# Kernel tuning notes

Hardware: AMD Instinct MI355X
Metric: run time of the kernel (lower is better)

Reference implementation:

```python
import jax, jax.numpy as jnp
import numpy as np

N = 200          # fixed by map_norm's .view(200, 1)
D = 8192         # in_features
EPS = 1e-5


def setup_inputs() -> dict:
    key = jax.random.key(0)
    ks = jax.random.split(key, 7)
    lim = float(np.sqrt(6.0 / D))
    x = jax.random.normal(ks[0], (N, D), dtype=jnp.float32)
    Wq = jax.random.uniform(ks[1], (D, D), dtype=jnp.float32, minval=-lim, maxval=lim)
    Wk = jax.random.uniform(ks[2], (D, D), dtype=jnp.float32, minval=-lim, maxval=lim)
    Wv = jax.random.uniform(ks[3], (D, D), dtype=jnp.float32, minval=-lim, maxval=lim)
    bq = jax.random.normal(ks[4], (D,), dtype=jnp.float32) * 0.01
    bk = jax.random.normal(ks[5], (D,), dtype=jnp.float32) * 0.01
    bv = jax.random.normal(ks[6], (D,), dtype=jnp.float32) * 0.01
    return {"x": x, "Wq": Wq, "bq": bq, "Wk": Wk, "bk": bk, "Wv": Wv, "bv": bv}


def reference(x, Wq, bq, Wk, bk, Wv, bv):
    d_out = x.shape[1]
    cc = jnp.sqrt(jnp.asarray(d_out, dtype=x.dtype))
    # nn.Linear: y = x @ W.T + b
    q = x @ Wq.T + bq          # [N, D]
    k = x @ Wk.T + bk          # [N, D]
    v = x @ Wv.T + bv          # [N, D]
    s = q @ k.T                # [N, N] score map
    mean = jnp.mean(s, axis=-1, keepdims=True)
    var = jnp.var(s, axis=-1, keepdims=True, ddof=1)  # torch.var is unbiased
    s = (s - mean) / jnp.sqrt(var + EPS)
    s = jnp.sin(s)
    scores = jax.nn.softmax(s / cc, axis=-1)
    return scores @ v          # [N, D]
```

## Files before the change

kernel.cpp:

```cpp
#include <hip/hip_runtime.h>
#include <hip/hip_bf16.h>
#include <cstdint>

#define DD 8192
#define NROW 200
#define MT 13
#define MPAD 208
#define KPV 256
#define EPSV 1e-5f
#define BK 64
#define ABUF_BYTES (MPAD * BK * 2)

using short8 = __attribute__((ext_vector_type(8))) short;
using f32x4  = __attribute__((ext_vector_type(4))) float;

#define MEMBAR asm volatile("" ::: "memory")
#define RAWBAR asm volatile("s_barrier" ::: "memory")

__device__ __forceinline__ ushort f2bf(float f) {
    union { float f; unsigned u; } c; c.f = f;
    unsigned u = c.u;
    return (ushort)((u + 0x7FFFu + ((u >> 16) & 1u)) >> 16);
}

__device__ __forceinline__ short8 pack8(float4 a, float4 b) {
    short8 o;
    o[0]=f2bf(a.x); o[1]=f2bf(a.y); o[2]=f2bf(a.z); o[3]=f2bf(a.w);
    o[4]=f2bf(b.x); o[5]=f2bf(b.y); o[6]=f2bf(b.z); o[7]=f2bf(b.w);
    return o;
}

__global__ void cvt_x(const float* __restrict__ x, ushort* __restrict__ xb) {
    int i = (blockIdx.x * 256 + threadIdx.x) * 8;
    int row = i >> 13;
    int col = i & (DD - 1);
    short8 o;
    if (row < NROW) {
        const float4* p = reinterpret_cast<const float4*>(x + (size_t)row * DD + col);
        float4 a = p[0], b = p[1];
        o = pack8(a, b);
    } else {
        for (int j = 0; j < 8; ++j) o[j] = 0;
    }
    *reinterpret_cast<short8*>(xb + i) = o;
}

__global__ __launch_bounds__(128) void qkv_gemm(
    const ushort* __restrict__ xb,
    const float* __restrict__ Wq, const float* __restrict__ Wk, const float* __restrict__ Wv,
    const float* __restrict__ bq, const float* __restrict__ bk, const float* __restrict__ bv,
    ushort* __restrict__ qb, ushort* __restrict__ kb, ushort* __restrict__ vt)
{
    __shared__ char Asm[2 * ABUF_BYTES];

    const int mat = blockIdx.y;
    const float* W    = (mat == 0) ? Wq : (mat == 1 ? Wk : Wv);
    const float* bias = (mat == 0) ? bq : (mat == 1 ? bk : bv);

    const int t     = threadIdx.x;
    const int lane  = t & 63;
    const int wave  = t >> 6;
    const int col16 = lane & 15;
    const int kgrp  = lane >> 4;
    const int ncol  = blockIdx.x * 32 + wave * 16 + col16;

    const float* wp = W + (size_t)ncol * DD + kgrp * 8;

    const ushort* sbase = xb + (size_t)(t >> 3) * DD + (size_t)(((t & 7) ^ ((t >> 3) & 7)) * 8);
    char* dbase = Asm + wave * 1024;

    const int b0off = col16 * 128 + ((kgrp ^ (col16 & 7)) * 16);
    const int b1off = b0off ^ 64;

    f32x4 acc[MT];
    #pragma unroll
    for (int m = 0; m < MT; ++m)
        for (int r = 0; r < 4; ++r) acc[m][r] = 0.f;

#define STAGE(B, KK) { _Pragma("unroll") for (int r = 0; r < 13; ++r) { \
        __builtin_amdgcn_global_load_lds( \
            (const __attribute__((address_space(1))) void*)(sbase + (KK) + r * 16 * DD), \
            (__attribute__((address_space(3))) void*)(dbase + (B) * ABUF_BYTES + r * 2048), \
            16, 0, 0); } }

#define LOADW(d0, d1, d2, d3, KK) { \
        d0 = *reinterpret_cast<const float4*>(wp + (KK)); \
        d1 = *reinterpret_cast<const float4*>(wp + (KK) + 4); \
        d2 = *reinterpret_cast<const float4*>(wp + (KK) + 32); \
        d3 = *reinterpret_cast<const float4*>(wp + (KK) + 36); }

#define COMPUTE(BASE, bb0, bb1) { \
        _Pragma("unroll") for (int m = 0; m < MT; ++m) { \
            short8 a0 = *reinterpret_cast<const short8*>(Asm + (BASE) + b0off + m * 2048); \
            acc[m] = __builtin_amdgcn_mfma_f32_16x16x32_bf16(a0, bb0, acc[m], 0, 0, 0); \
            short8 a1 = *reinterpret_cast<const short8*>(Asm + (BASE) + b1off + m * 2048); \
            acc[m] = __builtin_amdgcn_mfma_f32_16x16x32_bf16(a1, bb1, acc[m], 0, 0, 0); } }

    float4 wA0, wA1, wA2, wA3, wB0, wB1, wB2, wB3;

    STAGE(0, 0);
    MEMBAR;
    LOADW(wA0, wA1, wA2, wA3, 0);
    LOADW(wB0, wB1, wB2, wB3, BK);
    MEMBAR;

    for (int k0 = 0; k0 < DD; k0 += 2 * BK) {
        {
            short8 bb0 = pack8(wA0, wA1);
            short8 bb1 = pack8(wA2, wA3);
            STAGE(1, k0 + BK);
            MEMBAR;
            int kp = (k0 + 2 * BK) & (DD - 1);
            LOADW(wA0, wA1, wA2, wA3, kp);
            MEMBAR;
            asm volatile("s_waitcnt vmcnt(21)" ::: "memory");
            RAWBAR;
            COMPUTE(0, bb0, bb1);
            RAWBAR;
        }
        {
            short8 bb0 = pack8(wB0, wB1);
            short8 bb1 = pack8(wB2, wB3);
            int kp1 = (k0 + 2 * BK) & (DD - 1);
            STAGE(0, kp1);
            MEMBAR;
            int kp2 = (k0 + 3 * BK) & (DD - 1);
            LOADW(wB0, wB1, wB2, wB3, kp2);
            MEMBAR;
            asm volatile("s_waitcnt vmcnt(21)" ::: "memory");
            RAWBAR;
            COMPUTE(ABUF_BYTES, bb0, bb1);
            RAWBAR;
        }
    }
#undef STAGE
#undef LOADW
#undef COMPUTE

    const float badd = bias[ncol];
    if (mat < 2) {
        ushort* outb = (mat == 0) ? qb : kb;
        #pragma unroll
        for (int m = 0; m < MT; ++m)
            for (int r = 0; r < 4; ++r) {
                int row = m * 16 + kgrp * 4 + r;
                outb[(size_t)row * DD + ncol] = f2bf(acc[m][r] + badd);
            }
    } else {
        #pragma unroll
        for (int m = 0; m < MT; ++m)
            for (int r = 0; r < 4; ++r) {
                int row = m * 16 + kgrp * 4 + r;
                vt[(size_t)ncol * KPV + row] = f2bf(acc[m][r] + badd);
            }
    }
}

__global__ __launch_bounds__(256) void sgemm(const ushort* __restrict__ qb, const ushort* __restrict__ kb,
                                             float* __restrict__ sbuf) {
    const int bm = blockIdx.y, bn = blockIdx.x;
    const int lane  = threadIdx.x & 63;
    const int wave  = threadIdx.x >> 6;
    const int col16 = lane & 15, kgrp = lane >> 4;
    const ushort* ap = qb + (size_t)(bm * 16 + col16) * DD + kgrp * 8;
    const ushort* bp = kb + (size_t)(bn * 16 + col16) * DD + kgrp * 8;
    f32x4 acc;
    for (int r = 0; r < 4; ++r) acc[r] = 0.f;
    const int kend = (wave + 1) * 2048;
    for (int k0 = wave * 2048; k0 < kend; k0 += 32) {
        short8 a = *reinterpret_cast<const short8*>(ap + k0);
        short8 b = *reinterpret_cast<const short8*>(bp + k0);
        acc = __builtin_amdgcn_mfma_f32_16x16x32_bf16(a, b, acc, 0, 0, 0);
    }
    __shared__ f32x4 red[4][64];
    red[wave][lane] = acc;
    __syncthreads();
    if (wave == 0) {
        f32x4 s = red[0][lane];
        for (int j = 1; j < 4; ++j) { f32x4 o = red[j][lane]; for (int r = 0; r < 4; ++r) s[r] += o[r]; }
        for (int r = 0; r < 4; ++r)
            sbuf[(size_t)(bm * 16 + kgrp * 4 + r) * MPAD + bn * 16 + col16] = s[r];
    }
}

__global__ __launch_bounds__(256) void rownorm(const float* __restrict__ sbuf, ushort* __restrict__ pb) {
    const int row = blockIdx.x;
    const int t = threadIdx.x;
    if (row >= NROW) { pb[(size_t)row * KPV + t] = 0; return; }
    __shared__ float part[4];
    const int lane = t & 63, wave = t >> 6;
    float x = (t < NROW) ? sbuf[(size_t)row * MPAD + t] : 0.f;

    float s = x;
    for (int m = 32; m; m >>= 1) s += __shfl_xor(s, m, 64);
    if (lane == 0) part[wave] = s;
    __syncthreads();
    float mean = (part[0] + part[1] + part[2] + part[3]) * (1.f / 200.f);

    float d = (t < NROW) ? (x - mean) : 0.f;
    float s2 = d * d;
    for (int m = 32; m; m >>= 1) s2 += __shfl_xor(s2, m, 64);
    __syncthreads();
    if (lane == 0) part[wave] = s2;
    __syncthreads();
    float var = (part[0] + part[1] + part[2] + part[3]) * (1.f / 199.f);

    float inv = 1.f / sqrtf(var + EPSV);
    float y = sinf(d * inv);
    const float inv_cc = 1.f / 90.50966799187809f;
    float e = (t < NROW) ? expf(y * inv_cc) : 0.f;

    float se = e;
    for (int m = 32; m; m >>= 1) se += __shfl_xor(se, m, 64);
    __syncthreads();
    if (lane == 0) part[wave] = se;
    __syncthreads();
    float tot = part[0] + part[1] + part[2] + part[3];
    pb[(size_t)row * KPV + t] = (t < NROW) ? f2bf(e / tot) : (ushort)0;
}

__global__ __launch_bounds__(256) void pv_gemm(const ushort* __restrict__ pb, const ushort* __restrict__ vt,
                                               float* __restrict__ out) {
    const int lane  = threadIdx.x & 63;
    const int wave  = threadIdx.x >> 6;
    const int col16 = lane & 15, kgrp = lane >> 4;
    const int ncol  = blockIdx.x * 64 + wave * 16 + col16;
    const ushort* ap = pb + (size_t)col16 * KPV + kgrp * 8;
    const ushort* bp = vt + (size_t)ncol  * KPV + kgrp * 8;
    f32x4 acc[MT];
    for (int m = 0; m < MT; ++m)
        for (int r = 0; r < 4; ++r) acc[m][r] = 0.f;
    for (int k0 = 0; k0 < KPV; k0 += 32) {
        short8 b = *reinterpret_cast<const short8*>(bp + k0);
        #pragma unroll
        for (int m = 0; m < MT; ++m) {
            short8 a = *reinterpret_cast<const short8*>(ap + (size_t)m * 16 * KPV + k0);
            acc[m] = __builtin_amdgcn_mfma_f32_16x16x32_bf16(a, b, acc[m], 0, 0, 0);
        }
    }
    for (int m = 0; m < MT; ++m)
        for (int r = 0; r < 4; ++r) {
            int row = m * 16 + kgrp * 4 + r;
            if (row < NROW) out[(size_t)row * DD + ncol] = acc[m][r];
        }
}

extern "C" void kernel_launch(void* const* d_in, const int* in_sizes, int n_in,
                              void* d_out, int out_size, void* d_ws, size_t ws_size,
                              hipStream_t stream) {
    const float* x  = (const float*)d_in[0];
    const float* Wq = (const float*)d_in[1];
    const float* bq = (const float*)d_in[2];
    const float* Wk = (const float*)d_in[3];
    const float* bk = (const float*)d_in[4];
    const float* Wv = (const float*)d_in[5];
    const float* bv = (const float*)d_in[6];
    float* out = (float*)d_out;

    char* ws = (char*)d_ws;
    ushort* xb   = (ushort*)(ws);
    ushort* qb   = (ushort*)(ws + 3407872);
    ushort* kb   = (ushort*)(ws + 6815744);
    ushort* vt   = (ushort*)(ws + 10223616);
    float*  sbuf = (float*)(ws + 14417920);
    ushort* pb   = (ushort*)(ws + 14590976);

    cvt_x<<<832, 256, 0, stream>>>(x, xb);
    qkv_gemm<<<dim3(256, 3), 128, 0, stream>>>(xb, Wq, Wk, Wv, bq, bk, bv, qb, kb, vt);
    sgemm<<<dim3(13, 13), 256, 0, stream>>>(qb, kb, sbuf);
    rownorm<<<208, 256, 0, stream>>>(sbuf, pb);
    pv_gemm<<<128, 256, 0, stream>>>(pb, vt, out);
}
```

Before: 295.4 us.

## Make QKV GEMM single-wave per block computing two column tiles, drop barriers

The QKV projection kernel now launches one wave per block instead of two. That wave stages the whole 208x64 A tile itself and computes both 16-column groups, so each LDS A fragment feeds two MFMAs. With only one wave per block, the s_barrier pairs around each compute phase are removed and the vmcnt threshold is raised to match the larger number of loads in flight. The trade-off is twice the accumulator and weight registers per wave and half as many resident waves on the GPU, which may weaken latency hiding for the weight stream.

```diff
diff --git a/kernel.cpp b/kernel.cpp
--- a/kernel.cpp
+++ b/kernel.cpp
@@ -15,7 +15,6 @@
 using f32x4  = __attribute__((ext_vector_type(4))) float;
 
 #define MEMBAR asm volatile("" ::: "memory")
-#define RAWBAR asm volatile("s_barrier" ::: "memory")
 
 __device__ __forceinline__ ushort f2bf(float f) {
     union { float f; unsigned u; } c; c.f = f;
@@ -45,7 +44,7 @@
     *reinterpret_cast<short8*>(xb + i) = o;
 }
 
-__global__ __launch_bounds__(128) void qkv_gemm(
+__global__ __launch_bounds__(64) void qkv_gemm(
     const ushort* __restrict__ xb,
     const float* __restrict__ Wq, const float* __restrict__ Wk, const float* __restrict__ Wv,
     const float* __restrict__ bq, const float* __restrict__ bk, const float* __restrict__ bv,
@@ -57,101 +56,112 @@
     const float* W    = (mat == 0) ? Wq : (mat == 1 ? Wk : Wv);
     const float* bias = (mat == 0) ? bq : (mat == 1 ? bk : bv);
 
-    const int t     = threadIdx.x;
-    const int lane  = t & 63;
-    const int wave  = t >> 6;
+    const int lane  = threadIdx.x;
     const int col16 = lane & 15;
     const int kgrp  = lane >> 4;
-    const int ncol  = blockIdx.x * 32 + wave * 16 + col16;
-
-    const float* wp = W + (size_t)ncol * DD + kgrp * 8;
-
-    const ushort* sbase = xb + (size_t)(t >> 3) * DD + (size_t)(((t & 7) ^ ((t >> 3) & 7)) * 8);
-    char* dbase = Asm + wave * 1024;
+    const int ncol0 = blockIdx.x * 32 + col16;
+    const int ncol1 = ncol0 + 16;
+
+    const float* wp0 = W + (size_t)ncol0 * DD + kgrp * 8;
+    const float* wp1 = W + (size_t)ncol1 * DD + kgrp * 8;
+
+    const ushort* sbase = xb + (size_t)(lane >> 3) * DD
+                             + (size_t)(((lane & 7) ^ ((lane >> 3) & 7)) * 8);
 
     const int b0off = col16 * 128 + ((kgrp ^ (col16 & 7)) * 16);
     const int b1off = b0off ^ 64;
 
-    f32x4 acc[MT];
+    f32x4 acc0[MT], acc1[MT];
     #pragma unroll
     for (int m = 0; m < MT; ++m)
-        for (int r = 0; r < 4; ++r) acc[m][r] = 0.f;
-
-#define STAGE(B, KK) { _Pragma("unroll") for (int r = 0; r < 13; ++r) { \
+        for (int r = 0; r < 4; ++r) { acc0[m][r] = 0.f; acc1[m][r] = 0.f; }
+
+#define STAGE(B, KK) { _Pragma("unroll") for (int r = 0; r < 26; ++r) { \
         __builtin_amdgcn_global_load_lds( \
-            (const __attribute__((address_space(1))) void*)(sbase + (KK) + r * 16 * DD), \
-            (__attribute__((address_space(3))) void*)(dbase + (B) * ABUF_BYTES + r * 2048), \
+            (const __attribute__((address_space(1))) void*)(sbase + (KK) + r * 8 * DD), \
+            (__attribute__((address_space(3))) void*)(Asm + (B) * ABUF_BYTES + r * 1024), \
             16, 0, 0); } }
 
-#define LOADW(d0, d1, d2, d3, KK) { \
-        d0 = *reinterpret_cast<const float4*>(wp + (KK)); \
-        d1 = *reinterpret_cast<const float4*>(wp + (KK) + 4); \
-        d2 = *reinterpret_cast<const float4*>(wp + (KK) + 32); \
-        d3 = *reinterpret_cast<const float4*>(wp + (KK) + 36); }
-
-#define COMPUTE(BASE, bb0, bb1) { \
+#define LOADW(d, KK) { \
+        d##0 = *reinterpret_cast<const float4*>(wp0 + (KK)); \
+        d##1 = *reinterpret_cast<const float4*>(wp0 + (KK) + 4); \
+        d##2 = *reinterpret_cast<const float4*>(wp0 + (KK) + 32); \
+        d##3 = *reinterpret_cast<const float4*>(wp0 + (KK) + 36); \
+        d##4 = *reinterpret_cast<const float4*>(wp1 + (KK)); \
+        d##5 = *reinterpret_cast<const float4*>(wp1 + (KK) + 4); \
+        d##6 = *reinterpret_cast<const float4*>(wp1 + (KK) + 32); \
+        d##7 = *reinterpret_cast<const float4*>(wp1 + (KK) + 36); }
+
+#define COMPUTE(BASE, b00, b01, b10, b11) { \
         _Pragma("unroll") for (int m = 0; m < MT; ++m) { \
             short8 a0 = *reinterpret_cast<const short8*>(Asm + (BASE) + b0off + m * 2048); \
-            acc[m] = __builtin_amdgcn_mfma_f32_16x16x32_bf16(a0, bb0, acc[m], 0, 0, 0); \
+            acc0[m] = __builtin_amdgcn_mfma_f32_16x16x32_bf16(a0, b00, acc0[m], 0, 0, 0); \
+            acc1[m] = __builtin_amdgcn_mfma_f32_16x16x32_bf16(a0, b10, acc1[m], 0, 0, 0); \
             short8 a1 = *reinterpret_cast<const short8*>(Asm + (BASE) + b1off + m * 2048); \
-            acc[m] = __builtin_amdgcn_mfma_f32_16x16x32_bf16(a1, bb1, acc[m], 0, 0, 0); } }
-
-    float4 wA0, wA1, wA2, wA3, wB0, wB1, wB2, wB3;
+            acc0[m] = __builtin_amdgcn_mfma_f32_16x16x32_bf16(a1, b01, acc0[m], 0, 0, 0); \
+            acc1[m] = __builtin_amdgcn_mfma_f32_16x16x32_bf16(a1, b11, acc1[m], 0, 0, 0); } }
+
+    float4 wA0, wA1, wA2, wA3, wA4, wA5, wA6, wA7;
+    float4 wB0, wB1, wB2, wB3, wB4, wB5, wB6, wB7;
 
     STAGE(0, 0);
     MEMBAR;
-    LOADW(wA0, wA1, wA2, wA3, 0);
-    LOADW(wB0, wB1, wB2, wB3, BK);
+    LOADW(wA, 0);
+    MEMBAR;
+    LOADW(wB, BK);
     MEMBAR;
 
     for (int k0 = 0; k0 < DD; k0 += 2 * BK) {
         {
-            short8 bb0 = pack8(wA0, wA1);
-            short8 bb1 = pack8(wA2, wA3);
+            short8 b00 = pack8(wA0, wA1);
+            short8 b01 = pack8(wA2, wA3);
+            short8 b10 = pack8(wA4, wA5);
+            short8 b11 = pack8(wA6, wA7);
             STAGE(1, k0 + BK);
             MEMBAR;
             int kp = (k0 + 2 * BK) & (DD - 1);
-            LOADW(wA0, wA1, wA2, wA3, kp);
-            MEMBAR;
-            asm volatile("s_waitcnt vmcnt(21)" ::: "memory");
-            RAWBAR;
-            COMPUTE(0, bb0, bb1);
-            RAWBAR;
+            LOADW(wA, kp);
+            MEMBAR;
+            asm volatile("s_waitcnt vmcnt(42)" ::: "memory");
+            COMPUTE(0, b00, b01, b10, b11);
         }
         {
-            short8 bb0 = pack8(wB0, wB1);
-            short8 bb1 = pack8(wB2, wB3);
+            short8 b00 = pack8(wB0, wB1);
+            short8 b01 = pack8(wB2, wB3);
+            short8 b10 = pack8(wB4, wB5);
+            short8 b11 = pack8(wB6, wB7);
             int kp1 = (k0 + 2 * BK) & (DD - 1);
             STAGE(0, kp1);
             MEMBAR;
             int kp2 = (k0 + 3 * BK) & (DD - 1);
-            LOADW(wB0, wB1, wB2, wB3, kp2);
-            MEMBAR;
-            asm volatile("s_waitcnt vmcnt(21)" ::: "memory");
-            RAWBAR;
-            COMPUTE(ABUF_BYTES, bb0, bb1);
-            RAWBAR;
+            LOADW(wB, kp2);
+            MEMBAR;
+            asm volatile("s_waitcnt vmcnt(42)" ::: "memory");
+            COMPUTE(ABUF_BYTES, b00, b01, b10, b11);
         }
     }
 #undef STAGE
 #undef LOADW
 #undef COMPUTE
 
-    const float badd = bias[ncol];
+    const float badd0 = bias[ncol0];
+    const float badd1 = bias[ncol1];
     if (mat < 2) {
         ushort* outb = (mat == 0) ? qb : kb;
         #pragma unroll
         for (int m = 0; m < MT; ++m)
             for (int r = 0; r < 4; ++r) {
                 int row = m * 16 + kgrp * 4 + r;
-                outb[(size_t)row * DD + ncol] = f2bf(acc[m][r] + badd);
+                outb[(size_t)row * DD + ncol0] = f2bf(acc0[m][r] + badd0);
+                outb[(size_t)row * DD + ncol1] = f2bf(acc1[m][r] + badd1);
             }
     } else {
         #pragma unroll
         for (int m = 0; m < MT; ++m)
             for (int r = 0; r < 4; ++r) {
                 int row = m * 16 + kgrp * 4 + r;
-                vt[(size_t)ncol * KPV + row] = f2bf(acc[m][r] + badd);
+                vt[(size_t)ncol0 * KPV + row] = f2bf(acc0[m][r] + badd0);
+                vt[(size_t)ncol1 * KPV + row] = f2bf(acc1[m][r] + badd1);
             }
     }
 }
@@ -266,7 +276,7 @@
     ushort* pb   = (ushort*)(ws + 14590976);
 
     cvt_x<<<832, 256, 0, stream>>>(x, xb);
-    qkv_gemm<<<dim3(256, 3), 128, 0, stream>>>(xb, Wq, Wk, Wv, bq, bk, bv, qb, kb, vt);
+    qkv_gemm<<<dim3(256, 3), 64, 0, stream>>>(xb, Wq, Wk, Wv, bq, bk, bv, qb, kb, vt);
     sgemm<<<dim3(13, 13), 256, 0, stream>>>(qb, kb, sbuf);
     rownorm<<<208, 256, 0, stream>>>(sbuf, pb);
     pv_gemm<<<128, 256, 0, stream>>>(pb, vt, out);
```

After: 284.2 us. 3.8% less time.
